# Kernel optimization log

Measured on AMD Instinct MI355X. Metric: run time of the kernel, lower is better.

Reference implementation:

```python
import jax, jax.numpy as jnp
import numpy as np

LN_EPS = 1e-5  # torch LayerNorm default


def setup_inputs() -> dict:
    key = jax.random.key(0)
    k1, k2, k3 = jax.random.split(key, 3)
    B, L, D = 8, 2048, 1024
    CS, CD = 8192, 16
    x = jax.random.normal(k1, (B, L, D), dtype=jnp.float32)
    # xavier_uniform for Linear(dim, codebook_dim): bound = sqrt(6/(fan_in+fan_out))
    bound = float(np.sqrt(6.0 / (D + CD)))
    W = jax.random.uniform(k2, (CD, D), dtype=jnp.float32, minval=-bound, maxval=bound)
    codebook = jax.random.normal(k3, (CS, CD), dtype=jnp.float32)
    return {"x": x, "W": W, "codebook": codebook}


def reference(x, W, codebook):
    # random projection: (B,L,D) @ (D,CD) -> (B,L,CD)
    z = jnp.einsum("bld,cd->blc", x, W)
    # LayerNorm over last dim, no affine
    mu = jnp.mean(z, axis=-1, keepdims=True)
    var = jnp.mean(jnp.square(z - mu), axis=-1, keepdims=True)
    z = (z - mu) / jnp.sqrt(var + LN_EPS)
    # squared euclidean distance via matmul decomposition (avoids (B,L,CS,CD) tensor):
    # ||z - c||^2 = ||z||^2 - 2 z.c + ||c||^2 ; argmin is identical to argmin of the norm
    z_sq = jnp.sum(jnp.square(z), axis=-1, keepdims=True)        # (B,L,1)
    c_sq = jnp.sum(jnp.square(codebook), axis=-1)                # (CS,)
    d2 = z_sq - 2.0 * jnp.einsum("blc,kc->blk", z, codebook) + c_sq  # (B,L,CS)
    codes = jnp.argmin(d2, axis=-1)                              # (B,L) int32
    return codes
```

## Files before the change

### kernel.cpp

```cpp
#include <hip/hip_runtime.h>
#include <math.h>

#define D      1024
#define CD     16
#define CS     8192
#define ROWS   16384
#define LN_EPS 1e-5f
#define KCHUNK 512
#define NCHUNK (CS / KCHUNK)

typedef __attribute__((ext_vector_type(8))) short short8;
typedef __attribute__((ext_vector_type(4))) float f32x4;

__device__ inline unsigned short bf16_rne(float v) {
    unsigned u = __float_as_uint(v);
    unsigned r = u + 0x7FFFu + ((u >> 16) & 1u);
    return (unsigned short)(r >> 16);
}
__device__ inline short8 ld8(const unsigned short* p) { return *(const short8*)p; }

__device__ inline void split3(float v, unsigned short& a, unsigned short& b, unsigned short& c) {
    unsigned u = __float_as_uint(v);
    unsigned r = u + 0x7FFFu + ((u >> 16) & 1u);
    a = (unsigned short)(r >> 16);
    float r1 = v - __uint_as_float(r & 0xFFFF0000u);
    unsigned u1 = __float_as_uint(r1);
    unsigned r1b = u1 + 0x7FFFu + ((u1 >> 16) & 1u);
    b = (unsigned short)(r1b >> 16);
    float r2 = r1 - __uint_as_float(r1b & 0xFFFF0000u);
    c = bf16_rne(r2);
}

__global__ __launch_bounds__(256) void pack_all(const float* __restrict__ W,
                                                const float* __restrict__ cb,
                                                unsigned short* __restrict__ wb,
                                                unsigned short* __restrict__ cbp,
                                                float* __restrict__ nhc)
{
    const int t = threadIdx.x;
    if (blockIdx.x < 32) {
        int k = blockIdx.x * 256 + t;
        const float* c = cb + (long)k * CD;
        unsigned short* o = cbp + (long)k * 48;
        float csq = 0.f;
        #pragma unroll
        for (int d = 0; d < 16; ++d) {
            float v = c[d];
            csq = fmaf(v, v, csq);
            unsigned short h0, h1, h2;
            split3(v, h0, h1, h2);
            o[d] = h0; o[16 + d] = h1; o[32 + d] = h2;
        }
        nhc[k] = -0.5f * csq;
    } else {
        int tid = (blockIdx.x - 32) * 256 + t;
        int gk   = tid / 192;
        int rem  = tid % 192;
        int term = rem >> 6;
        int L    = rem & 63;
        int n = L & 15, q = L >> 4;
        const float* src = W + n * D + gk * 32 + q * 8;
        unsigned short* dst = wb + (size_t)tid * 8;
        #pragma unroll
        for (int j = 0; j < 8; ++j) {
            unsigned short h0, h1, h2;
            split3(src[j], h0, h1, h2);
            dst[j] = term == 0 ? h0 : (term == 1 ? h1 : h2);
        }
    }
}

__global__ __launch_bounds__(256, 4) void proj_ln(const float* __restrict__ x,
                                                  const unsigned short* __restrict__ wb,
                                                  unsigned short* __restrict__ zp)
{
    __shared__ float part[3][64][4];
    const int t = threadIdx.x;
    const int L = t & 63;
    const int kq = t >> 6;
    const int rt = blockIdx.x;
    const int n = L & 15, q = L >> 4;

    const float* xrow = x + (size_t)(rt * 16 + n) * D + kq * 256 + q * 8;
    const unsigned short* wbase = wb + (size_t)(kq * 8) * 1536;

    f32x4 acc0 = {0.f, 0.f, 0.f, 0.f};
    f32x4 acc1 = {0.f, 0.f, 0.f, 0.f};
    #pragma unroll
    for (int kk = 0; kk < 8; ++kk) {
        float4 xa = *(const float4*)(xrow + kk * 32);
        float4 xb = *(const float4*)(xrow + kk * 32 + 4);
        const unsigned short* wp = wbase + (size_t)kk * 1536 + L * 8;
        short8 w0 = ld8(wp);
        short8 w1 = ld8(wp + 512);
        short8 w2 = ld8(wp + 1024);
        float vs[8] = {xa.x, xa.y, xa.z, xa.w, xb.x, xb.y, xb.z, xb.w};
        short8 x0, x1, x2;
        #pragma unroll
        for (int j = 0; j < 8; ++j) {
            unsigned short h0, h1, h2;
            split3(vs[j], h0, h1, h2);
            x0[j] = (short)h0; x1[j] = (short)h1; x2[j] = (short)h2;
        }
        acc0 = __builtin_amdgcn_mfma_f32_16x16x32_bf16(x0, w0, acc0, 0, 0, 0);
        acc1 = __builtin_amdgcn_mfma_f32_16x16x32_bf16(x0, w1, acc1, 0, 0, 0);
        acc0 = __builtin_amdgcn_mfma_f32_16x16x32_bf16(x1, w0, acc0, 0, 0, 0);
        acc1 = __builtin_amdgcn_mfma_f32_16x16x32_bf16(x1, w1, acc1, 0, 0, 0);
        acc0 = __builtin_amdgcn_mfma_f32_16x16x32_bf16(x0, w2, acc0, 0, 0, 0);
        acc1 = __builtin_amdgcn_mfma_f32_16x16x32_bf16(x2, w0, acc1, 0, 0, 0);
    }

    if (kq != 0) {
        #pragma unroll
        for (int r = 0; r < 4; ++r) part[kq - 1][L][r] = acc0[r] + acc1[r];
    }
    __syncthreads();
    if (kq == 0) {
        #pragma unroll
        for (int r = 0; r < 4; ++r) {
            float zv = acc0[r] + acc1[r] + part[0][L][r] + part[1][L][r] + part[2][L][r];
            float s = zv;
            for (int m = 1; m < 16; m <<= 1) s += __shfl_xor(s, m, 64);
            float mu = s * (1.f / 16.f);
            float dd = zv - mu;
            float v2 = dd * dd;
            for (int m = 1; m < 16; m <<= 1) v2 += __shfl_xor(v2, m, 64);
            float var = v2 * (1.f / 16.f);
            float zn = dd / sqrtf(var + LN_EPS);
            unsigned short h0, h1, h2;
            split3(zn, h0, h1, h2);
            unsigned short* zr = zp + (size_t)(rt * 16 + q * 4 + r) * 48;
            zr[n] = h0; zr[16 + n] = h1; zr[32 + n] = h2;
        }
    }
}

__global__ __launch_bounds__(512, 4) void dist_argmin(const unsigned short* __restrict__ zp,
                                                      const unsigned short* __restrict__ cbp,
                                                      const float* __restrict__ nhc,
                                                      float* __restrict__ pbest,
                                                      int* __restrict__ pidx)
{
    __shared__ __align__(16) unsigned short cl[KCHUNK * 48];
    __shared__ float ql[KCHUNK];
    const int t = threadIdx.x;
    const int kbase = blockIdx.y * KCHUNK;

    {
        float4* dst = (float4*)cl;
        const float4* src = (const float4*)(cbp + (size_t)kbase * 48);
        #pragma unroll
        for (int i = 0; i < 6; ++i) dst[t + i * 512] = src[t + i * 512];
        if (t < KCHUNK / 4) ((float4*)ql)[t] = ((const float4*)(nhc + kbase))[t];
    }
    __syncthreads();

    const int L = t & 63;
    const int w = t >> 6;
    const int n = L & 15;
    const int q = L >> 4;

    const int oa2 = (q * 8 + 16) & 31;
    const int oa3 = q < 2 ? 32 + q * 8 : (q - 2) * 8;
    const int ob3 = q < 2 ? q * 8 : 16 + q * 8;

    short8 a1[2], a2[2], a3[2];
    const int rt0 = blockIdx.x * 16 + w * 2;
    #pragma unroll
    for (int j = 0; j < 2; ++j) {
        const unsigned short* zr = zp + (size_t)((rt0 + j) * 16 + n) * 48;
        a1[j] = ld8(zr + q * 8);
        a2[j] = ld8(zr + oa2);
        a3[j] = ld8(zr + oa3);
    }

    float best[2][4];
    int   bi[2][4];
    #pragma unroll
    for (int j = 0; j < 2; ++j)
        #pragma unroll
        for (int r = 0; r < 4; ++r) { best[j][r] = -INFINITY; bi[j][r] = 0; }

    #pragma unroll 2
    for (int tt = 0; tt < KCHUNK / 16; ++tt) {
        const unsigned short* cb_t = cl + (size_t)(tt * 16 + n) * 48;
        short8 b1 = ld8(cb_t + q * 8);
        short8 b3 = ld8(cb_t + ob3);
        float bneg = ql[tt * 16 + n];
        f32x4 bias = {bneg, bneg, bneg, bneg};
        int code = kbase + tt * 16 + n;
        f32x4 acc[2];
        #pragma unroll
        for (int j = 0; j < 2; ++j)
            acc[j] = __builtin_amdgcn_mfma_f32_16x16x32_bf16(a1[j], b1, bias, 0, 0, 0);
        #pragma unroll
        for (int j = 0; j < 2; ++j)
            acc[j] = __builtin_amdgcn_mfma_f32_16x16x32_bf16(a2[j], b1, acc[j], 0, 0, 0);
        #pragma unroll
        for (int j = 0; j < 2; ++j)
            acc[j] = __builtin_amdgcn_mfma_f32_16x16x32_bf16(a3[j], b3, acc[j], 0, 0, 0);
        #pragma unroll
        for (int j = 0; j < 2; ++j)
            #pragma unroll
            for (int r = 0; r < 4; ++r)
                if (acc[j][r] > best[j][r]) { best[j][r] = acc[j][r]; bi[j][r] = code; }
    }

    #pragma unroll
    for (int mask = 1; mask < 16; mask <<= 1) {
        #pragma unroll
        for (int j = 0; j < 2; ++j)
            #pragma unroll
            for (int r = 0; r < 4; ++r) {
                float s2 = __shfl_xor(best[j][r], mask, 64);
                int   i2 = __shfl_xor(bi[j][r], mask, 64);
                if (s2 > best[j][r] || (s2 == best[j][r] && i2 < bi[j][r])) {
                    best[j][r] = s2; bi[j][r] = i2;
                }
            }
    }
    if (n == 0) {
        #pragma unroll
        for (int j = 0; j < 2; ++j)
            #pragma unroll
            for (int r = 0; r < 4; ++r) {
                int row = (rt0 + j) * 16 + q * 4 + r;
                pbest[(size_t)row * NCHUNK + blockIdx.y] = best[j][r];
                pidx [(size_t)row * NCHUNK + blockIdx.y] = bi[j][r];
            }
    }
}

__global__ __launch_bounds__(256) void merge_argmin(const float* __restrict__ pbest,
                                                    const int* __restrict__ pidx,
                                                    int* __restrict__ out)
{
    const long row = (long)blockIdx.x * 256 + threadIdx.x;
    float best = -INFINITY;
    int   bi   = 0;
    #pragma unroll
    for (int i = 0; i < NCHUNK; ++i) {
        float s = pbest[row * NCHUNK + i];
        if (s > best) { best = s; bi = pidx[row * NCHUNK + i]; }
    }
    out[row] = bi;
}

extern "C" void kernel_launch(void* const* d_in, const int* in_sizes, int n_in,
                              void* d_out, int out_size, void* d_ws, size_t ws_size,
                              hipStream_t stream)
{
    const float* x  = (const float*)d_in[0];
    const float* W  = (const float*)d_in[1];
    const float* cb = (const float*)d_in[2];
    int* out = (int*)d_out;

    char* ws = (char*)d_ws;
    unsigned short* zp  = (unsigned short*)ws;
    unsigned short* cbp = (unsigned short*)(ws + 0x180000);
    float* nhc  = (float*)(ws + 0x240000);
    unsigned short* wb = (unsigned short*)(ws + 0x248000);
    float* pbest = (float*)(ws + 0x260000);
    int*   pidx  = (int*)  (ws + 0x360000);

    pack_all<<<56, 256, 0, stream>>>(W, cb, wb, cbp, nhc);
    proj_ln <<<ROWS / 16, 256, 0, stream>>>(x, wb, zp);
    dist_argmin<<<dim3(ROWS / 256, NCHUNK), 512, 0, stream>>>(zp, cbp, nhc, pbest, pidx);
    merge_argmin<<<ROWS / 256, 256, 0, stream>>>(pbest, pidx, out);
}
```

Baseline: 137.7 us.

## Switch codebook scoring to 32x32x16 MFMA tiles with six split-term products

Replaces the 16x16x32 bf16 MFMA scoring loop, which used two row tiles per wave and three MFMAs each, with a single 32x32x16 MFMA tile per wave. The bf16 split-term cross products are now issued as six separate MFMAs over a 32-row by 32-code tile. Each codebook load from shared memory now covers 32 codes and the loop runs half as many iterations. The argmin reduction runs over 32 lanes with a new row mapping for stores. The 16-element accumulator raises register pressure, and the 32x32 MFMA has different throughput and latency characteristics.

```diff
diff --git a/kernel.cpp b/kernel.cpp
--- a/kernel.cpp
+++ b/kernel.cpp
@@ -11,6 +11,7 @@
 
 typedef __attribute__((ext_vector_type(8))) short short8;
 typedef __attribute__((ext_vector_type(4))) float f32x4;
+typedef __attribute__((ext_vector_type(16))) float f32x16;
 
 __device__ inline unsigned short bf16_rne(float v) {
     unsigned u = __float_as_uint(v);
@@ -157,77 +158,60 @@
 
     const int L = t & 63;
     const int w = t >> 6;
-    const int n = L & 15;
-    const int q = L >> 4;
-
-    const int oa2 = (q * 8 + 16) & 31;
-    const int oa3 = q < 2 ? 32 + q * 8 : (q - 2) * 8;
-    const int ob3 = q < 2 ? q * 8 : 16 + q * 8;
-
-    short8 a1[2], a2[2], a3[2];
-    const int rt0 = blockIdx.x * 16 + w * 2;
-    #pragma unroll
-    for (int j = 0; j < 2; ++j) {
-        const unsigned short* zr = zp + (size_t)((rt0 + j) * 16 + n) * 48;
-        a1[j] = ld8(zr + q * 8);
-        a2[j] = ld8(zr + oa2);
-        a3[j] = ld8(zr + oa3);
-    }
-
-    float best[2][4];
-    int   bi[2][4];
-    #pragma unroll
-    for (int j = 0; j < 2; ++j)
-        #pragma unroll
-        for (int r = 0; r < 4; ++r) { best[j][r] = -INFINITY; bi[j][r] = 0; }
+    const int c31 = L & 31;
+    const int half = L >> 5;
+
+    const int rt = blockIdx.x * 8 + w;
+    const unsigned short* zr = zp + (size_t)(rt * 32 + c31) * 48 + half * 8;
+    short8 a0 = ld8(zr);
+    short8 a1 = ld8(zr + 16);
+    short8 a2 = ld8(zr + 32);
+
+    float best[16];
+    int   bi[16];
+    #pragma unroll
+    for (int r = 0; r < 16; ++r) { best[r] = -INFINITY; bi[r] = 0; }
 
     #pragma unroll 2
-    for (int tt = 0; tt < KCHUNK / 16; ++tt) {
-        const unsigned short* cb_t = cl + (size_t)(tt * 16 + n) * 48;
-        short8 b1 = ld8(cb_t + q * 8);
-        short8 b3 = ld8(cb_t + ob3);
-        float bneg = ql[tt * 16 + n];
-        f32x4 bias = {bneg, bneg, bneg, bneg};
-        int code = kbase + tt * 16 + n;
-        f32x4 acc[2];
-        #pragma unroll
-        for (int j = 0; j < 2; ++j)
-            acc[j] = __builtin_amdgcn_mfma_f32_16x16x32_bf16(a1[j], b1, bias, 0, 0, 0);
-        #pragma unroll
-        for (int j = 0; j < 2; ++j)
-            acc[j] = __builtin_amdgcn_mfma_f32_16x16x32_bf16(a2[j], b1, acc[j], 0, 0, 0);
-        #pragma unroll
-        for (int j = 0; j < 2; ++j)
-            acc[j] = __builtin_amdgcn_mfma_f32_16x16x32_bf16(a3[j], b3, acc[j], 0, 0, 0);
-        #pragma unroll
-        for (int j = 0; j < 2; ++j)
-            #pragma unroll
-            for (int r = 0; r < 4; ++r)
-                if (acc[j][r] > best[j][r]) { best[j][r] = acc[j][r]; bi[j][r] = code; }
-    }
-
-    #pragma unroll
-    for (int mask = 1; mask < 16; mask <<= 1) {
-        #pragma unroll
-        for (int j = 0; j < 2; ++j)
-            #pragma unroll
-            for (int r = 0; r < 4; ++r) {
-                float s2 = __shfl_xor(best[j][r], mask, 64);
-                int   i2 = __shfl_xor(bi[j][r], mask, 64);
-                if (s2 > best[j][r] || (s2 == best[j][r] && i2 < bi[j][r])) {
-                    best[j][r] = s2; bi[j][r] = i2;
-                }
+    for (int tt = 0; tt < KCHUNK / 32; ++tt) {
+        const unsigned short* cp = cl + (size_t)(tt * 32 + c31) * 48 + half * 8;
+        short8 b0 = ld8(cp);
+        short8 b1 = ld8(cp + 16);
+        short8 b2 = ld8(cp + 32);
+        float bneg = ql[tt * 32 + c31];
+        int code = kbase + tt * 32 + c31;
+        f32x16 acc;
+        #pragma unroll
+        for (int r = 0; r < 16; ++r) acc[r] = bneg;
+        acc = __builtin_amdgcn_mfma_f32_32x32x16_bf16(a0, b0, acc, 0, 0, 0);
+        acc = __builtin_amdgcn_mfma_f32_32x32x16_bf16(a1, b1, acc, 0, 0, 0);
+        acc = __builtin_amdgcn_mfma_f32_32x32x16_bf16(a1, b0, acc, 0, 0, 0);
+        acc = __builtin_amdgcn_mfma_f32_32x32x16_bf16(a0, b1, acc, 0, 0, 0);
+        acc = __builtin_amdgcn_mfma_f32_32x32x16_bf16(a2, b0, acc, 0, 0, 0);
+        acc = __builtin_amdgcn_mfma_f32_32x32x16_bf16(a0, b2, acc, 0, 0, 0);
+        #pragma unroll
+        for (int r = 0; r < 16; ++r)
+            if (acc[r] > best[r]) { best[r] = acc[r]; bi[r] = code; }
+    }
+
+    #pragma unroll
+    for (int mask = 1; mask < 32; mask <<= 1) {
+        #pragma unroll
+        for (int r = 0; r < 16; ++r) {
+            float s2 = __shfl_xor(best[r], mask, 64);
+            int   i2 = __shfl_xor(bi[r], mask, 64);
+            if (s2 > best[r] || (s2 == best[r] && i2 < bi[r])) {
+                best[r] = s2; bi[r] = i2;
             }
-    }
-    if (n == 0) {
-        #pragma unroll
-        for (int j = 0; j < 2; ++j)
-            #pragma unroll
-            for (int r = 0; r < 4; ++r) {
-                int row = (rt0 + j) * 16 + q * 4 + r;
-                pbest[(size_t)row * NCHUNK + blockIdx.y] = best[j][r];
-                pidx [(size_t)row * NCHUNK + blockIdx.y] = bi[j][r];
-            }
+        }
+    }
+    if (c31 == 0) {
+        #pragma unroll
+        for (int r = 0; r < 16; ++r) {
+            int row = rt * 32 + (r & 3) + 8 * (r >> 2) + 4 * half;
+            pbest[(size_t)row * NCHUNK + blockIdx.y] = best[r];
+            pidx [(size_t)row * NCHUNK + blockIdx.y] = bi[r];
+        }
     }
 }
 
```

Measured after the change: 145.9 us. +6.0%, slower.

## Store packed codebook in MFMA-fragment order for conflict-free LDS reads

Applied to the files above, without the earlier changes.

The codebook packing kernel now writes each 16-code tile in fragment order: lane-contiguous 8-element groups for the hi/mid terms, then the low term. The main kernel can then read its B operands at simple base+tt*768 offsets instead of 96-byte strided rows, which should reduce LDS bank conflicts and address arithmetic. It also tracks the best tile index instead of the full code in the inner loop and rebuilds the code index afterwards. This adds a fragile coupling between the packing layout and the MFMA lane mapping.

```diff
diff --git a/kernel.cpp b/kernel.cpp
--- a/kernel.cpp
+++ b/kernel.cpp
@@ -41,15 +41,31 @@
     if (blockIdx.x < 32) {
         int k = blockIdx.x * 256 + t;
         const float* c = cb + (long)k * CD;
-        unsigned short* o = cbp + (long)k * 48;
+        int tile = k >> 4;
+        int n    = k & 15;
+        unsigned short* base = cbp + (size_t)tile * 768;
         float csq = 0.f;
+        unsigned short h0[16], h1[16], h2[16];
         #pragma unroll
         for (int d = 0; d < 16; ++d) {
             float v = c[d];
             csq = fmaf(v, v, csq);
-            unsigned short h0, h1, h2;
-            split3(v, h0, h1, h2);
-            o[d] = h0; o[16 + d] = h1; o[32 + d] = h2;
+            split3(v, h0[d], h1[d], h2[d]);
+        }
+        #pragma unroll
+        for (int qq = 0; qq < 4; ++qq) {
+            const unsigned short* src = (qq < 2 ? h0 : h1) + (qq & 1) * 8;
+            short8 v;
+            #pragma unroll
+            for (int j = 0; j < 8; ++j) v[j] = (short)src[j];
+            *(short8*)(base + qq * 128 + n * 8) = v;
+        }
+        #pragma unroll
+        for (int h = 0; h < 2; ++h) {
+            short8 v;
+            #pragma unroll
+            for (int j = 0; j < 8; ++j) v[j] = (short)h2[h * 8 + j];
+            *(short8*)(base + 512 + h * 128 + n * 8) = v;
         }
         nhc[k] = -0.5f * csq;
     } else {
@@ -162,7 +178,6 @@
 
     const int oa2 = (q * 8 + 16) & 31;
     const int oa3 = q < 2 ? 32 + q * 8 : (q - 2) * 8;
-    const int ob3 = q < 2 ? q * 8 : 16 + q * 8;
 
     short8 a1[2], a2[2], a3[2];
     const int rt0 = blockIdx.x * 16 + w * 2;
@@ -174,21 +189,22 @@
         a3[j] = ld8(zr + oa3);
     }
 
+    const unsigned short* b1base = cl + L * 8;
+    const unsigned short* b3base = cl + L * 8 + (L >= 32 ? 256 : 0);
+
     float best[2][4];
-    int   bi[2][4];
+    int   bt[2][4];
     #pragma unroll
     for (int j = 0; j < 2; ++j)
         #pragma unroll
-        for (int r = 0; r < 4; ++r) { best[j][r] = -INFINITY; bi[j][r] = 0; }
+        for (int r = 0; r < 4; ++r) { best[j][r] = -INFINITY; bt[j][r] = 0; }
 
     #pragma unroll 2
     for (int tt = 0; tt < KCHUNK / 16; ++tt) {
-        const unsigned short* cb_t = cl + (size_t)(tt * 16 + n) * 48;
-        short8 b1 = ld8(cb_t + q * 8);
-        short8 b3 = ld8(cb_t + ob3);
+        short8 b1 = ld8(b1base + tt * 768);
+        short8 b3 = ld8(b3base + tt * 768);
         float bneg = ql[tt * 16 + n];
         f32x4 bias = {bneg, bneg, bneg, bneg};
-        int code = kbase + tt * 16 + n;
         f32x4 acc[2];
         #pragma unroll
         for (int j = 0; j < 2; ++j)
@@ -203,8 +219,14 @@
         for (int j = 0; j < 2; ++j)
             #pragma unroll
             for (int r = 0; r < 4; ++r)
-                if (acc[j][r] > best[j][r]) { best[j][r] = acc[j][r]; bi[j][r] = code; }
-    }
+                if (acc[j][r] > best[j][r]) { best[j][r] = acc[j][r]; bt[j][r] = tt; }
+    }
+
+    int bi[2][4];
+    #pragma unroll
+    for (int j = 0; j < 2; ++j)
+        #pragma unroll
+        for (int r = 0; r < 4; ++r) bi[j][r] = kbase + bt[j][r] * 16 + n;
 
     #pragma unroll
     for (int mask = 1; mask < 16; mask <<= 1) {
```

Result: no change. 138.6 us (+0.7%).
